# Kernel optimization log

Measured on AMD Instinct MI355X. Metric: run time of the kernel, lower is better.

## Reference

```python
import jax, jax.numpy as jnp
import numpy as np

N = 50000          # nodes
E = 800000         # edges
IN_DIM = 64
HIDDEN = 128
HEADS = 4
HEAD_DIM = HIDDEN // HEADS
EDGE_DIM = 6       # NUM_EDGE_FEATURES
LAYERS = 2
NEG_SLOPE = 0.2    # PyG GATv2Conv default
BN_EPS = 1e-5


def setup_inputs() -> dict:
    key = jax.random.key(0)
    ks = jax.random.split(key, 16)
    s = 0.05
    return {
        "x": jax.random.normal(ks[0], (N, IN_DIM), jnp.float32),
        "edge_index": jax.random.randint(ks[1], (2, E), 0, N, jnp.int64),
        "edge_attr": jax.random.normal(ks[2], (E, EDGE_DIM), jnp.float32),
        # input projection
        "Wproj": jax.random.normal(ks[3], (IN_DIM, HIDDEN), jnp.float32) * s,
        "bproj": jnp.zeros((HIDDEN,), jnp.float32),
        # per-layer GATv2 params, stacked over layers
        "Wl": jax.random.normal(ks[4], (LAYERS, HIDDEN, HIDDEN), jnp.float32) * s,
        "bl": jnp.zeros((LAYERS, HIDDEN), jnp.float32),
        "Wr": jax.random.normal(ks[5], (LAYERS, HIDDEN, HIDDEN), jnp.float32) * s,
        "br": jnp.zeros((LAYERS, HIDDEN), jnp.float32),
        "We": jax.random.normal(ks[6], (LAYERS, EDGE_DIM, HIDDEN), jnp.float32) * s,
        "be": jnp.zeros((LAYERS, HIDDEN), jnp.float32),
        "att": jax.random.normal(ks[7], (LAYERS, HEADS, HEAD_DIM), jnp.float32) * s,
        "conv_bias": jnp.zeros((LAYERS, HIDDEN), jnp.float32),
        # BatchNorm affine params
        "gamma": jnp.ones((LAYERS, HIDDEN), jnp.float32),
        "beta": jnp.zeros((LAYERS, HIDDEN), jnp.float32),
    }


def _gatv2_layer(x, src, dst, edge_attr, Wl, bl, Wr, br, We, be, att, bias):
    # Linear projections of source / target node features: [N, H, C]
    xl = (x @ Wl + bl).reshape(N, HEADS, HEAD_DIM)
    xr = (x @ Wr + br).reshape(N, HEADS, HEAD_DIM)
    # Per-edge message: x_j (src, lin_l) + x_i (dst, lin_r) + edge embedding
    m = xl[src] + xr[dst] + (edge_attr @ We + be).reshape(E, HEADS, HEAD_DIM)
    m = jax.nn.leaky_relu(m, NEG_SLOPE)
    logits = jnp.einsum('ehc,hc->eh', m, att)  # [E, H]
    # segment softmax over edges sharing the same destination node
    seg_max = jax.ops.segment_max(logits, dst, num_segments=N)  # [N, H]
    p = jnp.exp(logits - seg_max[dst])
    denom = jax.ops.segment_sum(p, dst, num_segments=N)  # [N, H]
    alpha = p / denom[dst]
    # weighted scatter-add of transformed source features
    out = jax.ops.segment_sum(xl[src] * alpha[:, :, None], dst, num_segments=N)
    return out.reshape(N, HIDDEN) + bias


def _batch_norm(x, gamma, beta):
    mu = jnp.mean(x, axis=0)
    var = jnp.var(x, axis=0)
    return (x - mu) * jax.lax.rsqrt(var + BN_EPS) * gamma + beta


def reference(x, edge_index, edge_attr, Wproj, bproj, Wl, bl, Wr, br, We, be, att,
              conv_bias, gamma, beta):
    src, dst = edge_index[0], edge_index[1]
    h = jax.nn.relu(x @ Wproj + bproj)  # dropout is identity in eval
    for i in range(LAYERS):
        h = _gatv2_layer(h, src, dst, edge_attr, Wl[i], bl[i], Wr[i], br[i],
                         We[i], be[i], att[i], conv_bias[i])
        h = _batch_norm(h, gamma[i], beta[i])
        h = jax.nn.relu(h)
    return h
```

## Files before the change

### kernel.cpp

```cpp
#include <hip/hip_runtime.h>
#include <hip/hip_bf16.h>

#define NN 50000
#define EE 800000
#define IN_DIM 64
#define HIDDEN 128
#define HEADS 4
#define HEAD_DIM 32
#define EDGE_DIM 6
#define LAYERS 2
#define NEG_SLOPE 0.2f
#define BN_EPS 1e-5f

#define SCAN_CHUNK 1024
#define NSB ((NN + SCAN_CHUNK - 1) / SCAN_CHUNK)

__global__ void detect_layout(const int* __restrict__ ei, int* __restrict__ flag) {
    __shared__ int any;
    if (threadIdx.x == 0) any = 0;
    __syncthreads();
    int found = 0;
    #pragma unroll
    for (int k = 0; k < 16; ++k) {
        int e = threadIdx.x + k * 1024;
        if (ei[2 * e + 1] != 0) found = 1;
    }
    if (found) any = 1;
    __syncthreads();
    if (threadIdx.x == 0) *flag = any;
}

__global__ void normalize_edges(const int* __restrict__ ei, const int* __restrict__ flag,
                                int* __restrict__ src, int* __restrict__ dst) {
    int e = blockIdx.x * 256 + threadIdx.x;
    if (e >= EE) return;
    int s, d;
    if (*flag == 0) {
        s = ei[2 * e];
        d = ei[2 * EE + 2 * e];
    } else {
        s = ei[e];
        d = ei[EE + e];
    }
    s = (s < 0) ? 0 : ((s >= NN) ? NN - 1 : s);
    d = (d < 0) ? 0 : ((d >= NN) ? NN - 1 : d);
    src[e] = s;
    dst[e] = d;
}

__global__ void count_edges(const int* __restrict__ dst, int* __restrict__ counts) {
    int e = blockIdx.x * 256 + threadIdx.x;
    if (e < EE) atomicAdd(&counts[dst[e]], 1);
}

__global__ void scan_partial(const int* __restrict__ counts, int* __restrict__ bsum) {
    __shared__ int ws[4];
    const int tid = threadIdx.x;
    const int lane = tid & 63, wid = tid >> 6;
    int i0 = blockIdx.x * SCAN_CHUNK + tid * 4;
    int s = 0;
    #pragma unroll
    for (int k = 0; k < 4; ++k) {
        int i = i0 + k;
        if (i < NN) s += counts[i];
    }
    #pragma unroll
    for (int ofs = 1; ofs < 64; ofs <<= 1) s += __shfl_xor(s, ofs, 64);
    if (lane == 0) ws[wid] = s;
    __syncthreads();
    if (tid == 0) bsum[blockIdx.x] = ws[0] + ws[1] + ws[2] + ws[3];
}

__global__ void scan_bsum(int* __restrict__ bsum) {
    int lane = threadIdx.x;
    int v = (lane < NSB) ? bsum[lane] : 0;
    int x = v;
    #pragma unroll
    for (int ofs = 1; ofs < 64; ofs <<= 1) {
        int t = __shfl_up(x, ofs, 64);
        if (lane >= ofs) x += t;
    }
    if (lane < NSB) bsum[lane] = x - v;
}

__global__ void scan_final(const int* __restrict__ counts, const int* __restrict__ bsumX,
                           int* __restrict__ offsets, int* __restrict__ cursor) {
    __shared__ int ws[4];
    const int tid = threadIdx.x;
    const int lane = tid & 63, wid = tid >> 6;
    const int b = blockIdx.x;
    int i0 = b * SCAN_CHUNK + tid * 4;
    int v[4];
    int tsum = 0;
    #pragma unroll
    for (int k = 0; k < 4; ++k) {
        int i = i0 + k;
        v[k] = (i < NN) ? counts[i] : 0;
        tsum += v[k];
    }
    int x = tsum;
    #pragma unroll
    for (int ofs = 1; ofs < 64; ofs <<= 1) {
        int t = __shfl_up(x, ofs, 64);
        if (lane >= ofs) x += t;
    }
    if (lane == 63) ws[wid] = x;
    __syncthreads();
    int woff = 0;
    for (int w = 0; w < wid; ++w) woff += ws[w];
    int excl = (x - tsum) + woff + bsumX[b];
    #pragma unroll
    for (int k = 0; k < 4; ++k) {
        int i = i0 + k;
        if (i < NN) { offsets[i] = excl; cursor[i] = excl; }
        excl += v[k];
    }
    if (b == 0 && tid == 0) offsets[NN] = EE;
}

__global__ void bucket_edges(const int* __restrict__ dst, int* __restrict__ cursor,
                             int* __restrict__ sorted) {
    int e = blockIdx.x * 256 + threadIdx.x;
    if (e < EE) {
        int p = atomicAdd(&cursor[dst[e]], 1);
        sorted[p] = e;
    }
}

template <int K, bool RELU>
__launch_bounds__(256, 2)
__global__ void gemm_k(const float* __restrict__ A, const float* __restrict__ W,
                       const float* __restrict__ bias, float* __restrict__ out, int n) {
    constexpr int KC = 64;
    constexpr int NCH = K / KC;
    __shared__ float Ws[KC][128];
    __shared__ float As[32][KC];
    const int tid = threadIdx.x;
    const int tx = tid & 31;
    const int ty = tid >> 5;
    const int row0 = blockIdx.x * 32;

    float acc[4][4] = {};

    for (int ch = 0; ch < NCH; ++ch) {
        const float* Wp = W + ch * KC * 128;
        for (int i = tid * 4; i < KC * 128; i += 256 * 4)
            *(float4*)&((float*)Ws)[i] = *(const float4*)&Wp[i];
        for (int i = tid * 4; i < 32 * KC; i += 256 * 4) {
            int r = i / KC, c = i % KC;
            int gr = row0 + r;
            float4 v = {0.f, 0.f, 0.f, 0.f};
            if (gr < n) v = *(const float4*)&A[gr * K + ch * KC + c];
            *(float4*)&As[r][c] = v;
        }
        __syncthreads();

        #pragma unroll 4
        for (int k4 = 0; k4 < KC; k4 += 4) {
            float4 av4[4];
            float aa[4][4];
            #pragma unroll
            for (int i = 0; i < 4; ++i) av4[i] = *(float4*)&As[ty * 4 + i][k4];
            #pragma unroll
            for (int i = 0; i < 4; ++i) {
                aa[i][0] = av4[i].x; aa[i][1] = av4[i].y;
                aa[i][2] = av4[i].z; aa[i][3] = av4[i].w;
            }
            #pragma unroll
            for (int j = 0; j < 4; ++j) {
                float4 w = *(float4*)&Ws[k4 + j][tx * 4];
                #pragma unroll
                for (int i = 0; i < 4; ++i) {
                    acc[i][0] += aa[i][j] * w.x;
                    acc[i][1] += aa[i][j] * w.y;
                    acc[i][2] += aa[i][j] * w.z;
                    acc[i][3] += aa[i][j] * w.w;
                }
            }
        }
        __syncthreads();
    }

    float4 bv = *(const float4*)&bias[tx * 4];
    #pragma unroll
    for (int i = 0; i < 4; ++i) {
        int gr = row0 + ty * 4 + i;
        if (gr < n) {
            float4 o;
            o.x = acc[i][0] + bv.x;
            o.y = acc[i][1] + bv.y;
            o.z = acc[i][2] + bv.z;
            o.w = acc[i][3] + bv.w;
            if (RELU) {
                o.x = fmaxf(o.x, 0.f); o.y = fmaxf(o.y, 0.f);
                o.z = fmaxf(o.z, 0.f); o.w = fmaxf(o.w, 0.f);
            }
            *(float4*)&out[gr * 128 + tx * 4] = o;
        }
    }
}

__launch_bounds__(256, 2)
__global__ void gemm_dual(const float* __restrict__ A,
                          const float* __restrict__ W1, const float* __restrict__ b1,
                          const float* __restrict__ W2, const float* __restrict__ b2,
                          float* __restrict__ out1, float* __restrict__ out2, int n) {
    constexpr int K = 128, KC = 32;
    __shared__ float W1s[KC][128];
    __shared__ float W2s[KC][128];
    __shared__ float As[32][KC];
    const int tid = threadIdx.x;
    const int tx = tid & 31;
    const int ty = tid >> 5;
    const int row0 = blockIdx.x * 32;

    float acc1[4][4] = {}, acc2[4][4] = {};

    for (int ch = 0; ch < K / KC; ++ch) {
        const float* W1p = W1 + ch * KC * 128;
        const float* W2p = W2 + ch * KC * 128;
        for (int i = tid * 4; i < KC * 128; i += 256 * 4) {
            *(float4*)&((float*)W1s)[i] = *(const float4*)&W1p[i];
            *(float4*)&((float*)W2s)[i] = *(const float4*)&W2p[i];
        }
        {
            int i = tid * 4;
            int r = i / KC, c = i % KC;
            int gr = row0 + r;
            float4 v = {0.f, 0.f, 0.f, 0.f};
            if (gr < n) v = *(const float4*)&A[gr * K + ch * KC + c];
            *(float4*)&As[r][c] = v;
        }
        __syncthreads();

        #pragma unroll
        for (int k4 = 0; k4 < KC; k4 += 4) {
            float4 av4[4];
            float aa[4][4];
            #pragma unroll
            for (int i = 0; i < 4; ++i) av4[i] = *(float4*)&As[ty * 4 + i][k4];
            #pragma unroll
            for (int i = 0; i < 4; ++i) {
                aa[i][0] = av4[i].x; aa[i][1] = av4[i].y;
                aa[i][2] = av4[i].z; aa[i][3] = av4[i].w;
            }
            #pragma unroll
            for (int j = 0; j < 4; ++j) {
                float4 w1 = *(float4*)&W1s[k4 + j][tx * 4];
                float4 w2 = *(float4*)&W2s[k4 + j][tx * 4];
                #pragma unroll
                for (int i = 0; i < 4; ++i) {
                    acc1[i][0] += aa[i][j] * w1.x;
                    acc1[i][1] += aa[i][j] * w1.y;
                    acc1[i][2] += aa[i][j] * w1.z;
                    acc1[i][3] += aa[i][j] * w1.w;
                    acc2[i][0] += aa[i][j] * w2.x;
                    acc2[i][1] += aa[i][j] * w2.y;
                    acc2[i][2] += aa[i][j] * w2.z;
                    acc2[i][3] += aa[i][j] * w2.w;
                }
            }
        }
        __syncthreads();
    }

    float4 bv1 = *(const float4*)&b1[tx * 4];
    float4 bv2 = *(const float4*)&b2[tx * 4];
    #pragma unroll
    for (int i = 0; i < 4; ++i) {
        int gr = row0 + ty * 4 + i;
        if (gr < n) {
            float4 o1, o2;
            o1.x = acc1[i][0] + bv1.x; o1.y = acc1[i][1] + bv1.y;
            o1.z = acc1[i][2] + bv1.z; o1.w = acc1[i][3] + bv1.w;
            o2.x = acc2[i][0] + bv2.x; o2.y = acc2[i][1] + bv2.y;
            o2.z = acc2[i][2] + bv2.z; o2.w = acc2[i][3] + bv2.w;
            *(float4*)&out1[gr * 128 + tx * 4] = o1;
            *(float4*)&out2[gr * 128 + tx * 4] = o2;
        }
    }
}

__launch_bounds__(256, 4)
__global__ void gat_agg(const float* __restrict__ xl, const float* __restrict__ xr,
                        const float* __restrict__ edge_attr,
                        const int* __restrict__ src,
                        const int* __restrict__ sorted, const int* __restrict__ offsets,
                        const float* __restrict__ We, const float* __restrict__ be,
                        const float* __restrict__ att, const float* __restrict__ cbias,
                        float* __restrict__ y) {
    __shared__ float sWe[EDGE_DIM][128];
    __shared__ float sbe[128];
    __shared__ float satt[128];
    __shared__ float scb[128];
    const int tid = threadIdx.x;
    for (int i = tid; i < EDGE_DIM * 128; i += 256) ((float*)sWe)[i] = We[i];
    if (tid < 128) { sbe[tid] = be[tid]; satt[tid] = att[tid]; scb[tid] = cbias[tid]; }
    __syncthreads();

    const int wid = tid >> 6, lane = tid & 63;
    const int node = blockIdx.x * 4 + wid;
    if (node >= NN) return;

    const int c0 = lane * 2;
    float2 xrv  = *(const float2*)&xr[(size_t)node * 128 + c0];
    float2 attv = *(const float2*)&satt[c0];
    float2 bev  = *(const float2*)&sbe[c0];
    const float base0 = xrv.x + bev.x;
    const float base1 = xrv.y + bev.y;

    const int off = offsets[node];
    const int deg = offsets[node + 1] - off;

    float mA = -1e30f, dA = 0.f, aA0 = 0.f, aA1 = 0.f;
    float mB = -1e30f, dB = 0.f, aB0 = 0.f, aB1 = 0.f;

    for (int chunk = 0; chunk < deg; chunk += 64) {
        int i = chunk + lane;
        int eidL = 0, sL = 0;
        if (i < deg) { eidL = sorted[off + i]; sL = src[eidL]; }
        const int cnt = min(64, deg - chunk);

        for (int j = 0; j < cnt; j += 2) {
            const int j1 = (j + 1) & 63;
            int sa = __shfl(sL, j, 64);
            int ea = __shfl(eidL, j, 64);
            int sb = __shfl(sL, j1, 64);
            int eb = __shfl(eidL, j1, 64);
            float2 xa = *(const float2*)&xl[(size_t)sa * 128 + c0];
            float2 xb = *(const float2*)&xl[(size_t)sb * 128 + c0];
            const float* pa = &edge_attr[(size_t)ea * EDGE_DIM];
            const float* pb = &edge_attr[(size_t)eb * EDGE_DIM];
            float ma0 = xa.x + base0, ma1 = xa.y + base1;
            float mb0 = xb.x + base0, mb1 = xb.y + base1;
            #pragma unroll
            for (int k = 0; k < EDGE_DIM; ++k) {
                float2 w = *(const float2*)&sWe[k][c0];
                float va = pa[k], vb = pb[k];
                ma0 += va * w.x; ma1 += va * w.y;
                mb0 += vb * w.x; mb1 += vb * w.y;
            }
            ma0 = (ma0 > 0.f) ? ma0 : ma0 * NEG_SLOPE;
            ma1 = (ma1 > 0.f) ? ma1 : ma1 * NEG_SLOPE;
            mb0 = (mb0 > 0.f) ? mb0 : mb0 * NEG_SLOPE;
            mb1 = (mb1 > 0.f) ? mb1 : mb1 * NEG_SLOPE;
            float ta = ma0 * attv.x + ma1 * attv.y;
            float tb = mb0 * attv.x + mb1 * attv.y;
            #pragma unroll
            for (int ofs = 1; ofs <= 8; ofs <<= 1) {
                ta += __shfl_xor(ta, ofs, 64);
                tb += __shfl_xor(tb, ofs, 64);
            }
            {
                float nm = fmaxf(mA, ta);
                float sc = __expf(mA - nm);
                float p  = __expf(ta - nm);
                dA  = dA * sc + p;
                aA0 = aA0 * sc + p * xa.x;
                aA1 = aA1 * sc + p * xa.y;
                mA = nm;
            }
            if (j + 1 < cnt) {
                float nm = fmaxf(mB, tb);
                float sc = __expf(mB - nm);
                float p  = __expf(tb - nm);
                dB  = dB * sc + p;
                aB0 = aB0 * sc + p * xb.x;
                aB1 = aB1 * sc + p * xb.y;
                mB = nm;
            }
        }
    }

    float o0 = scb[c0], o1 = scb[c0 + 1];
    if (deg > 0) {
        float M  = fmaxf(mA, mB);
        float sA = __expf(mA - M);
        float sB = __expf(mB - M);
        float den = dA * sA + dB * sB;
        float inv = 1.f / den;
        o0 += (aA0 * sA + aB0 * sB) * inv;
        o1 += (aA1 * sA + aB1 * sB) * inv;
    }
    float2 r; r.x = o0; r.y = o1;
    *(float2*)&y[(size_t)node * 128 + c0] = r;
}

__global__ void bn_stats(const float* __restrict__ y, float* __restrict__ gsum,
                         float* __restrict__ gsq) {
    __shared__ float ls[128], lq[128];
    const int tid = threadIdx.x;
    if (tid < 128) { ls[tid] = 0.f; lq[tid] = 0.f; }
    __syncthreads();
    int idx = blockIdx.x * 256 + tid;
    const int stride = gridDim.x * 256;
    const int c4 = (idx & 31) * 4;
    float s[4] = {}, q[4] = {};
    for (; idx < NN * 32; idx += stride) {
        float4 v = ((const float4*)y)[idx];
        s[0] += v.x; q[0] += v.x * v.x;
        s[1] += v.y; q[1] += v.y * v.y;
        s[2] += v.z; q[2] += v.z * v.z;
        s[3] += v.w; q[3] += v.w * v.w;
    }
    #pragma unroll
    for (int j = 0; j < 4; ++j) {
        atomicAdd(&ls[c4 + j], s[j]);
        atomicAdd(&lq[c4 + j], q[j]);
    }
    __syncthreads();
    if (tid < 128) {
        atomicAdd(&gsum[tid], ls[tid]);
        atomicAdd(&gsq[tid],  lq[tid]);
    }
}

__global__ void bn_apply(const float* __restrict__ y, const float* __restrict__ gsum,
                         const float* __restrict__ gsq, const float* __restrict__ gamma,
                         const float* __restrict__ beta, float* __restrict__ out) {
    int idx = blockIdx.x * 256 + threadIdx.x;
    const int stride = gridDim.x * 256;
    const int c4 = (idx & 31) * 4;
    const float invN = 1.f / (float)NN;
    float sc[4], sh[4];
    #pragma unroll
    for (int j = 0; j < 4; ++j) {
        int c = c4 + j;
        float mu  = gsum[c] * invN;
        float var = fmaxf(gsq[c] * invN - mu * mu, 0.f);
        sc[j] = rsqrtf(var + BN_EPS) * gamma[c];
        sh[j] = beta[c] - mu * sc[j];
    }
    for (; idx < NN * 32; idx += stride) {
        float4 v = ((const float4*)y)[idx];
        float4 o;
        o.x = fmaxf(v.x * sc[0] + sh[0], 0.f);
        o.y = fmaxf(v.y * sc[1] + sh[1], 0.f);
        o.z = fmaxf(v.z * sc[2] + sh[2], 0.f);
        o.w = fmaxf(v.w * sc[3] + sh[3], 0.f);
        ((float4*)out)[idx] = o;
    }
}

extern "C" void kernel_launch(void* const* d_in, const int* in_sizes, int n_in,
                              void* d_out, int out_size, void* d_ws, size_t ws_size,
                              hipStream_t stream) {
    const float* x        = (const float*)d_in[0];
    const int*   eidx     = (const int*)d_in[1];
    const float* edge_attr= (const float*)d_in[2];
    const float* Wproj    = (const float*)d_in[3];
    const float* bproj    = (const float*)d_in[4];
    const float* Wl       = (const float*)d_in[5];
    const float* bl       = (const float*)d_in[6];
    const float* Wr       = (const float*)d_in[7];
    const float* br       = (const float*)d_in[8];
    const float* We       = (const float*)d_in[9];
    const float* be       = (const float*)d_in[10];
    const float* att      = (const float*)d_in[11];
    const float* cbias    = (const float*)d_in[12];
    const float* gamma    = (const float*)d_in[13];
    const float* beta     = (const float*)d_in[14];

    char* ws = (char*)d_ws;
    auto alloc = [&](size_t bytes) {
        char* p = ws;
        ws += (bytes + 255) & ~(size_t)255;
        return p;
    };
    float* h      = (float*)alloc((size_t)NN * 128 * 4);
    float* xlB    = (float*)alloc((size_t)NN * 128 * 4);
    float* xrB    = (float*)alloc((size_t)NN * 128 * 4);
    int*   srcN   = (int*)alloc((size_t)EE * 4);
    int*   dstN   = (int*)alloc((size_t)EE * 4);
    int*   counts = (int*)alloc((size_t)NN * 4);
    int*   offs   = (int*)alloc((size_t)(NN + 1) * 4);
    int*   cursor = (int*)alloc((size_t)NN * 4);
    int*   sorted = (int*)alloc((size_t)EE * 4);
    int*   bsum   = (int*)alloc((size_t)NSB * 4);
    int*   flag   = (int*)alloc(256);
    float* gsum   = (float*)alloc((size_t)LAYERS * 128 * 4);
    float* gsq    = (float*)alloc((size_t)LAYERS * 128 * 4);

    hipMemsetAsync(counts, 0, (size_t)NN * 4, stream);
    hipMemsetAsync(gsum, 0, (size_t)LAYERS * 128 * 4, stream);
    hipMemsetAsync(gsq,  0, (size_t)LAYERS * 128 * 4, stream);

    detect_layout<<<1, 1024, 0, stream>>>(eidx, flag);
    normalize_edges<<<(EE + 255) / 256, 256, 0, stream>>>(eidx, flag, srcN, dstN);

    count_edges<<<(EE + 255) / 256, 256, 0, stream>>>(dstN, counts);
    scan_partial<<<NSB, 256, 0, stream>>>(counts, bsum);
    scan_bsum<<<1, 64, 0, stream>>>(bsum);
    scan_final<<<NSB, 256, 0, stream>>>(counts, bsum, offs, cursor);
    bucket_edges<<<(EE + 255) / 256, 256, 0, stream>>>(dstN, cursor, sorted);

    gemm_k<IN_DIM, true><<<(NN + 31) / 32, 256, 0, stream>>>(x, Wproj, bproj, h, NN);

    for (int l = 0; l < LAYERS; ++l) {
        gemm_dual<<<(NN + 31) / 32, 256, 0, stream>>>(
            h,
            Wl + (size_t)l * 128 * 128, bl + l * 128,
            Wr + (size_t)l * 128 * 128, br + l * 128,
            xlB, xrB, NN);
        gat_agg<<<(NN + 3) / 4, 256, 0, stream>>>(
            xlB, xrB, edge_attr, srcN, sorted, offs,
            We + (size_t)l * EDGE_DIM * 128, be + l * 128, att + l * 128,
            cbias + l * 128, h);
        bn_stats<<<400, 256, 0, stream>>>(h, gsum + l * 128, gsq + l * 128);
        float* outp = (l == LAYERS - 1) ? (float*)d_out : h;
        bn_apply<<<512, 256, 0, stream>>>(h, gsum + l * 128, gsq + l * 128,
                                          gamma + l * 128, beta + l * 128, outp);
    }
}
```

Measured before the change: 647.7 us.

## Process four edges per wavefront in parallel with 16-lane groups in GAT aggregation

The per-node aggregation kernel now splits each 64-lane wavefront into four 16-lane groups. Each group handles one edge at a time, and each lane covers 8 channels with float4 loads. Each group keeps its own online-softmax state, and the four partial states are merged with cross-lane shuffles at the end. This gives four independent edge gathers in flight per wavefront instead of a serial two-edge loop. It also drops the per-chunk broadcast shuffles, at the cost of more registers per lane and idle groups when a node has few edges.

```diff
diff --git a/kernel.cpp b/kernel.cpp
--- a/kernel.cpp
+++ b/kernel.cpp
@@ -302,88 +302,108 @@
     const int node = blockIdx.x * 4 + wid;
     if (node >= NN) return;
 
-    const int c0 = lane * 2;
-    float2 xrv  = *(const float2*)&xr[(size_t)node * 128 + c0];
-    float2 attv = *(const float2*)&satt[c0];
-    float2 bev  = *(const float2*)&sbe[c0];
-    const float base0 = xrv.x + bev.x;
-    const float base1 = xrv.y + bev.y;
+    const int g  = lane >> 4;
+    const int gl = lane & 15;
+    const int c0 = gl * 8;
+
+    float4 xr0 = *(const float4*)&xr[(size_t)node * 128 + c0];
+    float4 xr1 = *(const float4*)&xr[(size_t)node * 128 + c0 + 4];
+    float4 at0 = *(const float4*)&satt[c0];
+    float4 at1 = *(const float4*)&satt[c0 + 4];
+    float4 be0 = *(const float4*)&sbe[c0];
+    float4 be1 = *(const float4*)&sbe[c0 + 4];
+    float4 b0, b1;
+    b0.x = xr0.x + be0.x; b0.y = xr0.y + be0.y; b0.z = xr0.z + be0.z; b0.w = xr0.w + be0.w;
+    b1.x = xr1.x + be1.x; b1.y = xr1.y + be1.y; b1.z = xr1.z + be1.z; b1.w = xr1.w + be1.w;
 
     const int off = offsets[node];
     const int deg = offsets[node + 1] - off;
 
-    float mA = -1e30f, dA = 0.f, aA0 = 0.f, aA1 = 0.f;
-    float mB = -1e30f, dB = 0.f, aB0 = 0.f, aB1 = 0.f;
-
-    for (int chunk = 0; chunk < deg; chunk += 64) {
-        int i = chunk + lane;
-        int eidL = 0, sL = 0;
-        if (i < deg) { eidL = sorted[off + i]; sL = src[eidL]; }
-        const int cnt = min(64, deg - chunk);
-
-        for (int j = 0; j < cnt; j += 2) {
-            const int j1 = (j + 1) & 63;
-            int sa = __shfl(sL, j, 64);
-            int ea = __shfl(eidL, j, 64);
-            int sb = __shfl(sL, j1, 64);
-            int eb = __shfl(eidL, j1, 64);
-            float2 xa = *(const float2*)&xl[(size_t)sa * 128 + c0];
-            float2 xb = *(const float2*)&xl[(size_t)sb * 128 + c0];
-            const float* pa = &edge_attr[(size_t)ea * EDGE_DIM];
-            const float* pb = &edge_attr[(size_t)eb * EDGE_DIM];
-            float ma0 = xa.x + base0, ma1 = xa.y + base1;
-            float mb0 = xb.x + base0, mb1 = xb.y + base1;
-            #pragma unroll
-            for (int k = 0; k < EDGE_DIM; ++k) {
-                float2 w = *(const float2*)&sWe[k][c0];
-                float va = pa[k], vb = pb[k];
-                ma0 += va * w.x; ma1 += va * w.y;
-                mb0 += vb * w.x; mb1 += vb * w.y;
-            }
-            ma0 = (ma0 > 0.f) ? ma0 : ma0 * NEG_SLOPE;
-            ma1 = (ma1 > 0.f) ? ma1 : ma1 * NEG_SLOPE;
-            mb0 = (mb0 > 0.f) ? mb0 : mb0 * NEG_SLOPE;
-            mb1 = (mb1 > 0.f) ? mb1 : mb1 * NEG_SLOPE;
-            float ta = ma0 * attv.x + ma1 * attv.y;
-            float tb = mb0 * attv.x + mb1 * attv.y;
-            #pragma unroll
-            for (int ofs = 1; ofs <= 8; ofs <<= 1) {
-                ta += __shfl_xor(ta, ofs, 64);
-                tb += __shfl_xor(tb, ofs, 64);
-            }
-            {
-                float nm = fmaxf(mA, ta);
-                float sc = __expf(mA - nm);
-                float p  = __expf(ta - nm);
-                dA  = dA * sc + p;
-                aA0 = aA0 * sc + p * xa.x;
-                aA1 = aA1 * sc + p * xa.y;
-                mA = nm;
-            }
-            if (j + 1 < cnt) {
-                float nm = fmaxf(mB, tb);
-                float sc = __expf(mB - nm);
-                float p  = __expf(tb - nm);
-                dB  = dB * sc + p;
-                aB0 = aB0 * sc + p * xb.x;
-                aB1 = aB1 * sc + p * xb.y;
-                mB = nm;
-            }
-        }
-    }
-
-    float o0 = scb[c0], o1 = scb[c0 + 1];
-    if (deg > 0) {
-        float M  = fmaxf(mA, mB);
-        float sA = __expf(mA - M);
-        float sB = __expf(mB - M);
-        float den = dA * sA + dB * sB;
-        float inv = 1.f / den;
-        o0 += (aA0 * sA + aB0 * sB) * inv;
-        o1 += (aA1 * sA + aB1 * sB) * inv;
-    }
-    float2 r; r.x = o0; r.y = o1;
-    *(float2*)&y[(size_t)node * 128 + c0] = r;
+    float m = -1e30f, d = 0.f;
+    float4 a0 = {0.f, 0.f, 0.f, 0.f}, a1 = {0.f, 0.f, 0.f, 0.f};
+
+    for (int base = 0; base < deg; base += 4) {
+        const int idx  = base + g;
+        const int cidx = (idx < deg) ? idx : deg - 1;
+        const int eid = sorted[off + cidx];
+        const int s   = src[eid];
+        const float* xp = &xl[(size_t)s * 128 + c0];
+        float4 x0 = *(const float4*)xp;
+        float4 x1 = *(const float4*)(xp + 4);
+        const float* pe = &edge_attr[(size_t)eid * EDGE_DIM];
+
+        float4 m0, m1;
+        m0.x = x0.x + b0.x; m0.y = x0.y + b0.y; m0.z = x0.z + b0.z; m0.w = x0.w + b0.w;
+        m1.x = x1.x + b1.x; m1.y = x1.y + b1.y; m1.z = x1.z + b1.z; m1.w = x1.w + b1.w;
+        #pragma unroll
+        for (int k = 0; k < EDGE_DIM; ++k) {
+            float v = pe[k];
+            float4 w0 = *(const float4*)&sWe[k][c0];
+            float4 w1 = *(const float4*)&sWe[k][c0 + 4];
+            m0.x += v * w0.x; m0.y += v * w0.y; m0.z += v * w0.z; m0.w += v * w0.w;
+            m1.x += v * w1.x; m1.y += v * w1.y; m1.z += v * w1.z; m1.w += v * w1.w;
+        }
+        m0.x = (m0.x > 0.f) ? m0.x : m0.x * NEG_SLOPE;
+        m0.y = (m0.y > 0.f) ? m0.y : m0.y * NEG_SLOPE;
+        m0.z = (m0.z > 0.f) ? m0.z : m0.z * NEG_SLOPE;
+        m0.w = (m0.w > 0.f) ? m0.w : m0.w * NEG_SLOPE;
+        m1.x = (m1.x > 0.f) ? m1.x : m1.x * NEG_SLOPE;
+        m1.y = (m1.y > 0.f) ? m1.y : m1.y * NEG_SLOPE;
+        m1.z = (m1.z > 0.f) ? m1.z : m1.z * NEG_SLOPE;
+        m1.w = (m1.w > 0.f) ? m1.w : m1.w * NEG_SLOPE;
+
+        float t = m0.x * at0.x + m0.y * at0.y + m0.z * at0.z + m0.w * at0.w
+                + m1.x * at1.x + m1.y * at1.y + m1.z * at1.z + m1.w * at1.w;
+        t += __shfl_xor(t, 1, 64);
+        t += __shfl_xor(t, 2, 64);
+
+        if (idx < deg) {
+            float nm = fmaxf(m, t);
+            float sc = __expf(m - nm);
+            float p  = __expf(t - nm);
+            d = d * sc + p;
+            a0.x = a0.x * sc + p * x0.x; a0.y = a0.y * sc + p * x0.y;
+            a0.z = a0.z * sc + p * x0.z; a0.w = a0.w * sc + p * x0.w;
+            a1.x = a1.x * sc + p * x1.x; a1.y = a1.y * sc + p * x1.y;
+            a1.z = a1.z * sc + p * x1.z; a1.w = a1.w * sc + p * x1.w;
+            m = nm;
+        }
+    }
+
+    #pragma unroll
+    for (int ofs = 16; ofs <= 32; ofs <<= 1) {
+        float mo = __shfl_xor(m, ofs, 64);
+        float do_ = __shfl_xor(d, ofs, 64);
+        float4 p0, p1;
+        p0.x = __shfl_xor(a0.x, ofs, 64); p0.y = __shfl_xor(a0.y, ofs, 64);
+        p0.z = __shfl_xor(a0.z, ofs, 64); p0.w = __shfl_xor(a0.w, ofs, 64);
+        p1.x = __shfl_xor(a1.x, ofs, 64); p1.y = __shfl_xor(a1.y, ofs, 64);
+        p1.z = __shfl_xor(a1.z, ofs, 64); p1.w = __shfl_xor(a1.w, ofs, 64);
+        float M  = fmaxf(m, mo);
+        float s1 = __expf(m - M);
+        float s2 = __expf(mo - M);
+        d = d * s1 + do_ * s2;
+        a0.x = a0.x * s1 + p0.x * s2; a0.y = a0.y * s1 + p0.y * s2;
+        a0.z = a0.z * s1 + p0.z * s2; a0.w = a0.w * s1 + p0.w * s2;
+        a1.x = a1.x * s1 + p1.x * s2; a1.y = a1.y * s1 + p1.y * s2;
+        a1.z = a1.z * s1 + p1.z * s2; a1.w = a1.w * s1 + p1.w * s2;
+        m = M;
+    }
+
+    if (g == 0) {
+        float4 cb0 = *(const float4*)&scb[c0];
+        float4 cb1 = *(const float4*)&scb[c0 + 4];
+        float4 o0 = cb0, o1 = cb1;
+        if (deg > 0) {
+            float inv = 1.f / d;
+            o0.x += a0.x * inv; o0.y += a0.y * inv;
+            o0.z += a0.z * inv; o0.w += a0.w * inv;
+            o1.x += a1.x * inv; o1.y += a1.y * inv;
+            o1.z += a1.z * inv; o1.w += a1.w * inv;
+        }
+        *(float4*)&y[(size_t)node * 128 + c0]     = o0;
+        *(float4*)&y[(size_t)node * 128 + c0 + 4] = o1;
+    }
 }
 
 __global__ void bn_stats(const float* __restrict__ y, float* __restrict__ gsum,
```

Result: slower. 947.6 us (+46.3%).

## Store xl and edge attributes as bf16, pre-sort src/attrs by destination

Applied to the files above, without the earlier changes.

The bucketing pass now writes the source index and bf16-packed edge attributes directly in destination-sorted order. This removes the indirection through the sorted edge-id array and the scattered edge_attr reads in the aggregation kernel. The xl projection is stored as bf16, halving the bytes of the random per-edge gather, and gat_agg's occupancy hint rises to 8 blocks. The cost is lower precision in the messages and the aggregated values, plus extra scattered writes in the bucketing pass.

```diff
diff --git a/kernel.cpp b/kernel.cpp
--- a/kernel.cpp
+++ b/kernel.cpp
@@ -14,6 +14,14 @@
 
 #define SCAN_CHUNK 1024
 #define NSB ((NN + SCAN_CHUNK - 1) / SCAN_CHUNK)
+
+__device__ __forceinline__ unsigned bf2pack(float a, float b) {
+    unsigned ua = __float_as_uint(a); ua = (ua + 0x7FFFu + ((ua >> 16) & 1u)) >> 16;
+    unsigned ub = __float_as_uint(b); ub = (ub + 0x7FFFu + ((ub >> 16) & 1u)) >> 16;
+    return ua | (ub << 16);
+}
+__device__ __forceinline__ float bf_lo(unsigned u) { return __uint_as_float(u << 16); }
+__device__ __forceinline__ float bf_hi(unsigned u) { return __uint_as_float(u & 0xFFFF0000u); }
 
 __global__ void detect_layout(const int* __restrict__ ei, int* __restrict__ flag) {
     __shared__ int any;
@@ -118,12 +126,18 @@
     if (b == 0 && tid == 0) offsets[NN] = EE;
 }
 
-__global__ void bucket_edges(const int* __restrict__ dst, int* __restrict__ cursor,
-                             int* __restrict__ sorted) {
+__global__ void bucket_edges(const int* __restrict__ dst, const int* __restrict__ srcN,
+                             const float* __restrict__ ea, int* __restrict__ cursor,
+                             int* __restrict__ ssrc, unsigned* __restrict__ eattr_s) {
     int e = blockIdx.x * 256 + threadIdx.x;
     if (e < EE) {
         int p = atomicAdd(&cursor[dst[e]], 1);
-        sorted[p] = e;
+        ssrc[p] = srcN[e];
+        const float* a = &ea[(size_t)e * EDGE_DIM];
+        unsigned* o = eattr_s + (size_t)p * 3;
+        o[0] = bf2pack(a[0], a[1]);
+        o[1] = bf2pack(a[2], a[3]);
+        o[2] = bf2pack(a[4], a[5]);
     }
 }
 
@@ -204,7 +218,8 @@
 __global__ void gemm_dual(const float* __restrict__ A,
                           const float* __restrict__ W1, const float* __restrict__ b1,
                           const float* __restrict__ W2, const float* __restrict__ b2,
-                          float* __restrict__ out1, float* __restrict__ out2, int n) {
+                          unsigned short* __restrict__ out1, float* __restrict__ out2,
+                          int n) {
     constexpr int K = 128, KC = 32;
     __shared__ float W1s[KC][128];
     __shared__ float W2s[KC][128];
@@ -270,22 +285,26 @@
     for (int i = 0; i < 4; ++i) {
         int gr = row0 + ty * 4 + i;
         if (gr < n) {
-            float4 o1, o2;
-            o1.x = acc1[i][0] + bv1.x; o1.y = acc1[i][1] + bv1.y;
-            o1.z = acc1[i][2] + bv1.z; o1.w = acc1[i][3] + bv1.w;
+            float o1x = acc1[i][0] + bv1.x, o1y = acc1[i][1] + bv1.y;
+            float o1z = acc1[i][2] + bv1.z, o1w = acc1[i][3] + bv1.w;
+            float4 o2;
             o2.x = acc2[i][0] + bv2.x; o2.y = acc2[i][1] + bv2.y;
             o2.z = acc2[i][2] + bv2.z; o2.w = acc2[i][3] + bv2.w;
-            *(float4*)&out1[gr * 128 + tx * 4] = o1;
+            uint2 pk;
+            pk.x = bf2pack(o1x, o1y);
+            pk.y = bf2pack(o1z, o1w);
+            *(uint2*)&out1[gr * 128 + tx * 4] = pk;
             *(float4*)&out2[gr * 128 + tx * 4] = o2;
         }
     }
 }
 
-__launch_bounds__(256, 4)
-__global__ void gat_agg(const float* __restrict__ xl, const float* __restrict__ xr,
-                        const float* __restrict__ edge_attr,
-                        const int* __restrict__ src,
-                        const int* __restrict__ sorted, const int* __restrict__ offsets,
+__launch_bounds__(256, 8)
+__global__ void gat_agg(const unsigned short* __restrict__ xl,
+                        const float* __restrict__ xr,
+                        const unsigned* __restrict__ eattr_s,
+                        const int* __restrict__ ssrc,
+                        const int* __restrict__ offsets,
                         const float* __restrict__ We, const float* __restrict__ be,
                         const float* __restrict__ att, const float* __restrict__ cbias,
                         float* __restrict__ y) {
@@ -317,28 +336,35 @@
 
     for (int chunk = 0; chunk < deg; chunk += 64) {
         int i = chunk + lane;
-        int eidL = 0, sL = 0;
-        if (i < deg) { eidL = sorted[off + i]; sL = src[eidL]; }
+        int sL = 0;
+        if (i < deg) sL = ssrc[off + i];
         const int cnt = min(64, deg - chunk);
+        const unsigned* ep = eattr_s + (size_t)(off + chunk) * 3;
 
         for (int j = 0; j < cnt; j += 2) {
-            const int j1 = (j + 1) & 63;
+            const bool hb = (j + 1 < cnt);
+            const int jb = hb ? j + 1 : j;
             int sa = __shfl(sL, j, 64);
-            int ea = __shfl(eidL, j, 64);
-            int sb = __shfl(sL, j1, 64);
-            int eb = __shfl(eidL, j1, 64);
-            float2 xa = *(const float2*)&xl[(size_t)sa * 128 + c0];
-            float2 xb = *(const float2*)&xl[(size_t)sb * 128 + c0];
-            const float* pa = &edge_attr[(size_t)ea * EDGE_DIM];
-            const float* pb = &edge_attr[(size_t)eb * EDGE_DIM];
-            float ma0 = xa.x + base0, ma1 = xa.y + base1;
-            float mb0 = xb.x + base0, mb1 = xb.y + base1;
+            int sb = __shfl(sL, jb, 64);
+            unsigned xa_u = *(const unsigned*)&xl[(size_t)sa * 128 + c0];
+            unsigned xb_u = *(const unsigned*)&xl[(size_t)sb * 128 + c0];
+            unsigned ea0 = ep[j * 3], ea1 = ep[j * 3 + 1], ea2 = ep[j * 3 + 2];
+            unsigned eb0 = ep[jb * 3], eb1 = ep[jb * 3 + 1], eb2 = ep[jb * 3 + 2];
+
+            float xa0 = bf_lo(xa_u), xa1 = bf_hi(xa_u);
+            float xb0 = bf_lo(xb_u), xb1 = bf_hi(xb_u);
+            float eav[6] = {bf_lo(ea0), bf_hi(ea0), bf_lo(ea1),
+                            bf_hi(ea1), bf_lo(ea2), bf_hi(ea2)};
+            float ebv[6] = {bf_lo(eb0), bf_hi(eb0), bf_lo(eb1),
+                            bf_hi(eb1), bf_lo(eb2), bf_hi(eb2)};
+
+            float ma0 = xa0 + base0, ma1 = xa1 + base1;
+            float mb0 = xb0 + base0, mb1 = xb1 + base1;
             #pragma unroll
             for (int k = 0; k < EDGE_DIM; ++k) {
                 float2 w = *(const float2*)&sWe[k][c0];
-                float va = pa[k], vb = pb[k];
-                ma0 += va * w.x; ma1 += va * w.y;
-                mb0 += vb * w.x; mb1 += vb * w.y;
+                ma0 += eav[k] * w.x; ma1 += eav[k] * w.y;
+                mb0 += ebv[k] * w.x; mb1 += ebv[k] * w.y;
             }
             ma0 = (ma0 > 0.f) ? ma0 : ma0 * NEG_SLOPE;
             ma1 = (ma1 > 0.f) ? ma1 : ma1 * NEG_SLOPE;
@@ -356,17 +382,17 @@
                 float sc = __expf(mA - nm);
                 float p  = __expf(ta - nm);
                 dA  = dA * sc + p;
-                aA0 = aA0 * sc + p * xa.x;
-                aA1 = aA1 * sc + p * xa.y;
+                aA0 = aA0 * sc + p * xa0;
+                aA1 = aA1 * sc + p * xa1;
                 mA = nm;
             }
-            if (j + 1 < cnt) {
+            if (hb) {
                 float nm = fmaxf(mB, tb);
                 float sc = __expf(mB - nm);
                 float p  = __expf(tb - nm);
                 dB  = dB * sc + p;
-                aB0 = aB0 * sc + p * xb.x;
-                aB1 = aB1 * sc + p * xb.y;
+                aB0 = aB0 * sc + p * xb0;
+                aB1 = aB1 * sc + p * xb1;
                 mB = nm;
             }
         }
@@ -467,19 +493,20 @@
         ws += (bytes + 255) & ~(size_t)255;
         return p;
     };
-    float* h      = (float*)alloc((size_t)NN * 128 * 4);
-    float* xlB    = (float*)alloc((size_t)NN * 128 * 4);
-    float* xrB    = (float*)alloc((size_t)NN * 128 * 4);
-    int*   srcN   = (int*)alloc((size_t)EE * 4);
-    int*   dstN   = (int*)alloc((size_t)EE * 4);
-    int*   counts = (int*)alloc((size_t)NN * 4);
-    int*   offs   = (int*)alloc((size_t)(NN + 1) * 4);
-    int*   cursor = (int*)alloc((size_t)NN * 4);
-    int*   sorted = (int*)alloc((size_t)EE * 4);
-    int*   bsum   = (int*)alloc((size_t)NSB * 4);
-    int*   flag   = (int*)alloc(256);
-    float* gsum   = (float*)alloc((size_t)LAYERS * 128 * 4);
-    float* gsq    = (float*)alloc((size_t)LAYERS * 128 * 4);
+    float*          h      = (float*)alloc((size_t)NN * 128 * 4);
+    unsigned short* xlB    = (unsigned short*)alloc((size_t)NN * 128 * 2);
+    float*          xrB    = (float*)alloc((size_t)NN * 128 * 4);
+    int*            srcN   = (int*)alloc((size_t)EE * 4);
+    int*            dstN   = (int*)alloc((size_t)EE * 4);
+    int*            counts = (int*)alloc((size_t)NN * 4);
+    int*            offs   = (int*)alloc((size_t)(NN + 1) * 4);
+    int*            cursor = (int*)alloc((size_t)NN * 4);
+    int*            ssrc   = (int*)alloc((size_t)EE * 4);
+    unsigned*       eattrS = (unsigned*)alloc((size_t)EE * 12);
+    int*            bsum   = (int*)alloc((size_t)NSB * 4);
+    int*            flag   = (int*)alloc(256);
+    float*          gsum   = (float*)alloc((size_t)LAYERS * 128 * 4);
+    float*          gsq    = (float*)alloc((size_t)LAYERS * 128 * 4);
 
     hipMemsetAsync(counts, 0, (size_t)NN * 4, stream);
     hipMemsetAsync(gsum, 0, (size_t)LAYERS * 128 * 4, stream);
@@ -492,7 +519,8 @@
     scan_partial<<<NSB, 256, 0, stream>>>(counts, bsum);
     scan_bsum<<<1, 64, 0, stream>>>(bsum);
     scan_final<<<NSB, 256, 0, stream>>>(counts, bsum, offs, cursor);
-    bucket_edges<<<(EE + 255) / 256, 256, 0, stream>>>(dstN, cursor, sorted);
+    bucket_edges<<<(EE + 255) / 256, 256, 0, stream>>>(dstN, srcN, edge_attr,
+                                                       cursor, ssrc, eattrS);
 
     gemm_k<IN_DIM, true><<<(NN + 31) / 32, 256, 0, stream>>>(x, Wproj, bproj, h, NN);
 
@@ -503,7 +531,7 @@
             Wr + (size_t)l * 128 * 128, br + l * 128,
             xlB, xrB, NN);
         gat_agg<<<(NN + 3) / 4, 256, 0, stream>>>(
-            xlB, xrB, edge_attr, srcN, sorted, offs,
+            xlB, xrB, eattrS, ssrc, offs,
             We + (size_t)l * EDGE_DIM * 128, be + l * 128, att + l * 128,
             cbias + l * 128, h);
         bn_stats<<<400, 256, 0, stream>>>(h, gsum + l * 128, gsq + l * 128);
```

Result: slower. 823.0 us (+27.1%).
